# Kernel optimization log

Hardware: AMD Instinct MI355X
Metric: run time of the kernel (lower is better)

Reference implementation:

```python
import jax, jax.numpy as jnp
import numpy as np
import math

D_MODEL = 1024
N_HEAD = 16
D_HEAD = D_MODEL // N_HEAD
SCALE = math.sqrt(D_HEAD)
B, S = 8, 512


def setup_inputs() -> dict:
    key = jax.random.key(0)
    ks = jax.random.split(key, 7)
    x = jax.random.normal(ks[0], (B, S, D_MODEL), dtype=jnp.float32)
    mask = jnp.ones((B, S), dtype=jnp.int32)
    qmask = jax.random.randint(ks[1], (B, S), 0, 2).astype(jnp.int32)
    # params
    Wqkv = jax.random.normal(ks[2], (4 * D_MODEL, D_MODEL), dtype=jnp.float32) / math.sqrt(D_MODEL)
    fc_w = jax.random.normal(ks[3], (D_MODEL, D_MODEL), dtype=jnp.float32) / math.sqrt(D_MODEL)
    fc_b = jnp.zeros((D_MODEL,), dtype=jnp.float32)
    shift = jnp.abs(jax.random.normal(ks[4], (1,), dtype=jnp.float32)) + 0.001
    bias = -jnp.abs(jax.random.normal(ks[5], (1,), dtype=jnp.float32))
    return {"x": x, "mask": mask, "qmask": qmask, "Wqkv": Wqkv,
            "fc_w": fc_w, "fc_b": fc_b, "shift": shift, "bias": bias}


def reference(x, mask, qmask, Wqkv, fc_w, fc_b, shift, bias):
    Bsz, L, D = x.shape
    qkv = x @ Wqkv.T  # [B,S,4D], no bias
    q, k1, k2, v = jnp.split(qkv, 4, axis=-1)

    def heads(t):  # [B,S,D] -> [B,H,S,dh]
        return t.reshape(Bsz, L, N_HEAD, D_HEAD).transpose(0, 2, 1, 3)

    q, k1, k2, v = heads(q), heads(k1), heads(k2), heads(v)

    attn_self = jnp.einsum('bhqd,bhkd->bhqk', q, k1)
    attn_others = jnp.einsum('bhqd,bhkd->bhqk', q, k2)
    same_spk = (qmask[:, :, None] == qmask[:, None, :])[:, None]  # [B,1,S,S]
    attn = jnp.where(same_spk, attn_self, attn_others) / SCALE

    # key padding mask
    attn = jnp.where((mask == 0)[:, None, None, :], -jnp.inf, attn)

    # Gaussian distance bias: -(shift*(i-j)^2 + bias)
    pos = jnp.arange(L, dtype=jnp.float32)
    sq_dist = (pos[:, None] - pos[None, :]) ** 2  # [S,S]
    attn = attn - (shift[0] * sq_dist + bias[0])

    p = jax.nn.softmax(attn, axis=-1)  # dropout=0 (eval)
    out = jnp.einsum('bhqk,bhkd->bhqd', p, v)
    out = out.transpose(0, 2, 1, 3).reshape(Bsz, L, D)
    return out @ fc_w.T + fc_b
```

## Files before the change

kernel.cpp:

```cpp
#include <hip/hip_runtime.h>

typedef unsigned short u16;
typedef __bf16 bf16_t;
typedef bf16_t bf16x8 __attribute__((ext_vector_type(8)));
typedef float f32x4 __attribute__((ext_vector_type(4)));
typedef u16 u16x8 __attribute__((ext_vector_type(8)));
typedef u16 u16x4 __attribute__((ext_vector_type(4)));

__device__ __forceinline__ u16 f2b(float f) {
    unsigned int u = __float_as_uint(f);
    u += 0x7fffu + ((u >> 16) & 1u);
    return (u16)(u >> 16);
}
__device__ __forceinline__ unsigned int pk2(float a, float b) {
    return (unsigned int)f2b(a) | ((unsigned int)f2b(b) << 16);
}

__device__ __forceinline__ f32x4 mfma16(u16x8 a, u16x8 b, f32x4 c) {
    return __builtin_amdgcn_mfma_f32_16x16x32_bf16(
        __builtin_bit_cast(bf16x8, a), __builtin_bit_cast(bf16x8, b), c, 0, 0, 0);
}

#define GLDS16(gp, lp)                                                          \
    __builtin_amdgcn_global_load_lds(                                           \
        (const __attribute__((address_space(1))) void*)(gp),                    \
        (__attribute__((address_space(3))) void*)(lp), 16, 0, 0)

__global__ __launch_bounds__(256) void cvt3_kernel(const float* __restrict__ s0,
                                                   const float* __restrict__ s1,
                                                   const float* __restrict__ s2,
                                                   u16* __restrict__ d0,
                                                   u16* __restrict__ d1,
                                                   u16* __restrict__ d2) {
    int i = (blockIdx.x * 256 + threadIdx.x) * 4;
    const float* src; u16* dst;
    if (i < 4194304)       { src = s0;           dst = d0;           }
    else if (i < 8388608)  { src = s1 - 4194304; dst = d1 - 4194304; }
    else                   { src = s2 - 8388608; dst = d2 - 8388608; }
    float4 f = *(const float4*)(src + i);
    u16x4 o = { f2b(f.x), f2b(f.y), f2b(f.z), f2b(f.w) };
    *(u16x4*)(dst + i) = o;
}

template <int MT, int MODE>
__global__ __launch_bounds__(256) void gemm_bt(
    const u16* __restrict__ A, const u16* __restrict__ Bw,
    u16* __restrict__ Qf, u16* __restrict__ K1f,
    u16* __restrict__ K2f, u16* __restrict__ Vf,
    float* __restrict__ Cf, const float* __restrict__ biasp)
{
    constexpr int K = 1024;
    constexpr int MF = MT / 32;
    __shared__ u16 As[2][MT * 32];
    __shared__ u16 Bs[2][128 * 32];
    const int t = threadIdx.x;
    const int lane = t & 63;
    const int w = t >> 6;
    const int wm = w >> 1, wn = w & 1;
    const int lr = lane & 15, quad = lane >> 4;
    const int tileM = blockIdx.y * MT, tileN = blockIdx.x * 128;

    f32x4 acc[MF][4] = {};

    const u16* Ag = A + (size_t)(tileM + (t >> 2)) * K + (t & 3) * 8;
    const u16* Bg = Bw + (size_t)(tileN + (t >> 2)) * K + (t & 3) * 8;

    const bool swp = (MODE == 0) && (blockIdx.x < 24);
    const u16* Afb = swp ? &Bs[0][0] : &As[0][0];
    const u16* Bfb = swp ? &As[0][0] : &Bs[0][0];
    const int AfS = swp ? 128 * 32 : MT * 32;
    const int BfS = swp ? MT * 32 : 128 * 32;

#define STAGE(kk, bufi)                                                         \
    do {                                                                        \
        GLDS16(Ag + (kk), &As[bufi][t * 8]);                                    \
        if (MT == 128) GLDS16(Ag + (kk) + 64 * K, &As[bufi][t * 8 + 2048]);     \
        GLDS16(Bg + (kk), &Bs[bufi][t * 8]);                                    \
        GLDS16(Bg + (kk) + 64 * K, &Bs[bufi][t * 8 + 2048]);                    \
    } while (0)

    STAGE(0, 0);
    __syncthreads();

#pragma unroll 2
    for (int kk = 0; kk < K; kk += 32) {
        const int cur = (kk >> 5) & 1;
        if (kk + 32 < K) STAGE(kk + 32, cur ^ 1);

        u16x8 af[MF], bf[4];
#pragma unroll
        for (int i = 0; i < MF; ++i)
            af[i] = *(const u16x8*)(Afb + cur * AfS + (wm * (MT / 2) + i * 16 + lr) * 32 + quad * 8);
#pragma unroll
        for (int i = 0; i < 4; ++i)
            bf[i] = *(const u16x8*)(Bfb + cur * BfS + (wn * 64 + i * 16 + lr) * 32 + quad * 8);
#pragma unroll
        for (int mi = 0; mi < MF; ++mi)
#pragma unroll
            for (int ni = 0; ni < 4; ++ni)
                acc[mi][ni] = mfma16(af[mi], bf[ni], acc[mi][ni]);

        __syncthreads();
    }
#undef STAGE

    if (MODE == 0) {
        if (swp) {
            const int kvi = blockIdx.x >> 3;
            const int h = ((blockIdx.x & 7) << 1) + wm;
            const int bh = ((blockIdx.y >> 2) << 4) + h;
            const int t16b = ((blockIdx.y & 3) << 3) + wn * 4;
            u16* bp = (kvi == 0 ? Qf : (kvi == 1 ? K1f : K2f))
                    + ((size_t)(bh * 32 + t16b) * 2) * 512 + lr * 32 + quad * 4;
#pragma unroll
            for (int mi = 0; mi < MF; ++mi)
#pragma unroll
                for (int ni = 0; ni < 4; ++ni) {
                    uint2 v;
                    v.x = pk2(acc[mi][ni][0], acc[mi][ni][1]);
                    v.y = pk2(acc[mi][ni][2], acc[mi][ni][3]);
                    *(uint2*)(bp + ni * 1024 + (mi >> 1) * 512 + (mi & 1) * 16) = v;
                }
        } else {
            const int h = ((blockIdx.x - 24) << 1) + wn;
            const int bh = ((blockIdx.y >> 2) << 4) + h;
            const int t5b = ((blockIdx.y & 3) << 2) + wm * 2;
            u16* bp = Vf + ((size_t)(bh * 4) * 16 + t5b) * 512 + lr * 32 + quad * 4;
#pragma unroll
            for (int mi = 0; mi < MF; ++mi)
#pragma unroll
                for (int ni = 0; ni < 4; ++ni) {
                    uint2 v;
                    v.x = pk2(acc[mi][ni][0], acc[mi][ni][1]);
                    v.y = pk2(acc[mi][ni][2], acc[mi][ni][3]);
                    *(uint2*)(bp + ni * 8192 + (mi >> 1) * 512 + (mi & 1) * 16) = v;
                }
        }
    } else {
#pragma unroll
        for (int mi = 0; mi < MF; ++mi)
#pragma unroll
            for (int ni = 0; ni < 4; ++ni) {
                int n = tileN + wn * 64 + ni * 16 + lr;
                float bv = biasp[n];
#pragma unroll
                for (int r = 0; r < 4; ++r) {
                    int m = tileM + wm * (MT / 2) + mi * 16 + quad * 4 + r;
                    Cf[(size_t)m * 1024 + n] = acc[mi][ni][r] + bv;
                }
            }
    }
}

__global__ __launch_bounds__(256) void attn_kernel(
    const u16* __restrict__ qfm, const u16* __restrict__ k1fm,
    const u16* __restrict__ k2fm, const u16* __restrict__ vfm,
    const int* __restrict__ maskp, const int* __restrict__ qmaskp,
    const float* __restrict__ shiftp, const float* __restrict__ biasp,
    u16* __restrict__ ao)
{
    __shared__ u16 Pw[4][2][512];

    const int bh = blockIdx.x & 127, qt = blockIdx.x >> 7;
    const int b = bh >> 4, h = bh & 15;
    const int t = threadIdx.x, lane = t & 63, w = t >> 6;
    const int lr = lane & 15, quad = lane >> 4;
    const float shiftv = shiftp[0], biasv = biasp[0];

    const int qbase = qt * 128 + w * 32;
    const int m16 = qbase >> 4;
    const int loff = lr * 32 + quad * 8;

    const u16* qb = qfm + ((size_t)(bh * 32 + m16) * 2) * 512 + loff;
    u16x8 qa[2][2];
    qa[0][0] = *(const u16x8*)(qb);
    qa[0][1] = *(const u16x8*)(qb + 512);
    qa[1][0] = *(const u16x8*)(qb + 1024);
    qa[1][1] = *(const u16x8*)(qb + 1536);

    int qmr[2][4]; float rowf[2][4];
#pragma unroll
    for (int g = 0; g < 2; ++g)
#pragma unroll
        for (int r = 0; r < 4; ++r) {
            int m = qbase + g * 16 + quad * 4 + r;
            qmr[g][r] = qmaskp[b * 512 + m];
            rowf[g][r] = (float)m;
        }

    f32x4 o[2][4] = {};
    float lsum[2][4] = {};

    u16* pb[2] = { &Pw[w][0][0], &Pw[w][1][0] };
    const int wa0 = quad * 128 + (((lr >> 3) ^ quad) * 8) + (lr & 7);
    const int wa1 = quad * 128 + (((2 | (lr >> 3)) ^ quad) * 8) + (lr & 7);
    const int ra = lr * 32 + ((quad ^ (lr >> 2)) * 8);

    const u16* k1b = k1fm + (size_t)bh * 32768 + loff;
    const u16* k2b = k2fm + (size_t)bh * 32768 + loff;
    const u16* vb  = vfm  + (size_t)bh * 32768 + loff;
    const int* qmb = qmaskp + b * 512;
    const int* kmb = maskp + b * 512;

#pragma unroll 2
    for (int cc = 0; cc < 16; ++cc) {
        const u16* kc1 = k1b + cc * 2048;
        const u16* kc2 = k2b + cc * 2048;
        u16x8 k1f_[2][2], k2f_[2][2];
        k1f_[0][0] = *(const u16x8*)(kc1);
        k1f_[0][1] = *(const u16x8*)(kc1 + 512);
        k1f_[1][0] = *(const u16x8*)(kc1 + 1024);
        k1f_[1][1] = *(const u16x8*)(kc1 + 1536);
        k2f_[0][0] = *(const u16x8*)(kc2);
        k2f_[0][1] = *(const u16x8*)(kc2 + 512);
        k2f_[1][0] = *(const u16x8*)(kc2 + 1024);
        k2f_[1][1] = *(const u16x8*)(kc2 + 1536);
        u16x8 vf_[4];
#pragma unroll
        for (int ot = 0; ot < 4; ++ot)
            vf_[ot] = *(const u16x8*)(vb + (size_t)(ot * 16 + cc) * 512);

        f32x4 z = {0.f, 0.f, 0.f, 0.f};
        f32x4 s1[2][2], s2[2][2];
#pragma unroll
        for (int g = 0; g < 2; ++g)
#pragma unroll
            for (int tg = 0; tg < 2; ++tg) {
                s1[g][tg] = mfma16(qa[g][1], k1f_[tg][1], mfma16(qa[g][0], k1f_[tg][0], z));
                s2[g][tg] = mfma16(qa[g][1], k2f_[tg][1], mfma16(qa[g][0], k2f_[tg][0], z));
            }

        const int col0 = cc * 32 + lr, col1 = col0 + 16;
        const int qmc0 = qmb[col0], qmc1 = qmb[col1];
        const float ka0 = (kmb[col0] ? 0.f : -1e30f) - 10.0f;
        const float ka1 = (kmb[col1] ? 0.f : -1e30f) - 10.0f;
        const float colf0 = (float)col0, colf1 = (float)col1;

#pragma unroll
        for (int g = 0; g < 2; ++g) {
#pragma unroll
            for (int r = 0; r < 4; ++r) {
                float d0 = rowf[g][r] - colf0;
                float d1 = rowf[g][r] - colf1;
                float sel0 = (qmr[g][r] == qmc0) ? s1[g][0][r] : s2[g][0][r];
                float sel1 = (qmr[g][r] == qmc1) ? s1[g][1][r] : s2[g][1][r];
                float v0 = fmaf(sel0, 0.125f, -fmaf(shiftv * d0, d0, biasv)) + ka0;
                float v1 = fmaf(sel1, 0.125f, -fmaf(shiftv * d1, d1, biasv)) + ka1;
                float p0 = __expf(v0);
                float p1 = __expf(v1);
                lsum[g][r] += p0 + p1;
                pb[g][wa0 + r * 32] = f2b(p0);
                pb[g][wa1 + r * 32] = f2b(p1);
            }
        }
#pragma unroll
        for (int g = 0; g < 2; ++g) {
            u16x8 af = *(const u16x8*)(pb[g] + ra);
#pragma unroll
            for (int ot = 0; ot < 4; ++ot)
                o[g][ot] = mfma16(af, vf_[ot], o[g][ot]);
        }
    }

#pragma unroll
    for (int g = 0; g < 2; ++g)
#pragma unroll
        for (int r = 0; r < 4; ++r) {
            float s = lsum[g][r];
#pragma unroll
            for (int m = 1; m < 16; m <<= 1) s += __shfl_xor(s, m);
            float inv = 1.0f / s;
            int grow = b * 512 + qbase + g * 16 + quad * 4 + r;
            u16* orow = ao + (size_t)grow * 1024 + h * 64 + lr;
            orow[0]  = f2b(o[g][0][r] * inv);
            orow[16] = f2b(o[g][1][r] * inv);
            orow[32] = f2b(o[g][2][r] * inv);
            orow[48] = f2b(o[g][3][r] * inv);
        }
}

extern "C" void kernel_launch(void* const* d_in, const int* in_sizes, int n_in,
                              void* d_out, int out_size, void* d_ws, size_t ws_size,
                              hipStream_t stream) {
    (void)in_sizes; (void)n_in; (void)out_size; (void)ws_size;
    const float* x      = (const float*)d_in[0];
    const int*   maskp  = (const int*)d_in[1];
    const int*   qmaskp = (const int*)d_in[2];
    const float* Wqkv   = (const float*)d_in[3];
    const float* fc_w   = (const float*)d_in[4];
    const float* fc_b   = (const float*)d_in[5];
    const float* shiftp = (const float*)d_in[6];
    const float* biasp  = (const float*)d_in[7];
    float* out = (float*)d_out;

    char* ws = (char*)d_ws;
    u16* xb   = (u16*)(ws);
    u16* wb   = (u16*)(ws + (8u << 20));
    u16* fwb  = (u16*)(ws + (16u << 20));
    u16* qfm  = (u16*)(ws + (18u << 20));
    u16* k1fm = (u16*)(ws + (26u << 20));
    u16* k2fm = (u16*)(ws + (34u << 20));
    u16* vfm  = (u16*)(ws + (42u << 20));
    u16* aob  = (u16*)(ws + (50u << 20));

    cvt3_kernel<<<9216, 256, 0, stream>>>(x, Wqkv, fc_w, xb, wb, fwb);
    gemm_bt<128, 0><<<dim3(32, 32), 256, 0, stream>>>(xb, wb, qfm, k1fm, k2fm, vfm,
                                                      nullptr, nullptr);
    attn_kernel<<<512, 256, 0, stream>>>(qfm, k1fm, k2fm, vfm, maskp, qmaskp,
                                         shiftp, biasp, aob);
    gemm_bt<64, 1><<<dim3(8, 64), 256, 0, stream>>>(aob, fwb, nullptr, nullptr,
                                                    nullptr, nullptr, out, fc_b);
}
```

Before: 204.7 us.

## Replace direct global-to-LDS loads with register-staged double-buffered prefetch in GEMM

Tile loading in the bf16 GEMM changes from global_load_lds into LDS to ordinary global loads into registers, issued two K-steps ahead. The registers are then written to the alternate LDS buffer after each step's MFMAs. The aim is to hide global memory latency behind a deeper prefetch and to keep loads from sitting in the synchronisation path. In exchange it uses more VGPRs for the staging registers and adds explicit LDS store instructions, which may lower occupancy.

Result: no change. 206.2 us (+0.7%).

```diff
diff --git a/kernel.cpp b/kernel.cpp
--- a/kernel.cpp
+++ b/kernel.cpp
@@ -20,11 +20,6 @@
     return __builtin_amdgcn_mfma_f32_16x16x32_bf16(
         __builtin_bit_cast(bf16x8, a), __builtin_bit_cast(bf16x8, b), c, 0, 0, 0);
 }
-
-#define GLDS16(gp, lp)                                                          \
-    __builtin_amdgcn_global_load_lds(                                           \
-        (const __attribute__((address_space(1))) void*)(gp),                    \
-        (__attribute__((address_space(3))) void*)(lp), 16, 0, 0)
 
 __global__ __launch_bounds__(256) void cvt3_kernel(const float* __restrict__ s0,
                                                    const float* __restrict__ s1,
@@ -51,6 +46,7 @@
 {
     constexpr int K = 1024;
     constexpr int MF = MT / 32;
+    constexpr int NA = (MT == 128) ? 2 : 1;
     __shared__ u16 As[2][MT * 32];
     __shared__ u16 Bs[2][128 * 32];
     const int t = threadIdx.x;
@@ -71,38 +67,54 @@
     const int AfS = swp ? 128 * 32 : MT * 32;
     const int BfS = swp ? MT * 32 : 128 * 32;
 
-#define STAGE(kk, bufi)                                                         \
+    u16x8 rA[2][NA], rB[2][2];
+
+#define LOADR(kk, s)                                                            \
     do {                                                                        \
-        GLDS16(Ag + (kk), &As[bufi][t * 8]);                                    \
-        if (MT == 128) GLDS16(Ag + (kk) + 64 * K, &As[bufi][t * 8 + 2048]);     \
-        GLDS16(Bg + (kk), &Bs[bufi][t * 8]);                                    \
-        GLDS16(Bg + (kk) + 64 * K, &Bs[bufi][t * 8 + 2048]);                    \
+        rA[s][0] = *(const u16x8*)(Ag + (kk));                                  \
+        if (NA == 2) rA[s][NA - 1] = *(const u16x8*)(Ag + (kk) + 64 * K);       \
+        rB[s][0] = *(const u16x8*)(Bg + (kk));                                  \
+        rB[s][1] = *(const u16x8*)(Bg + (kk) + 64 * K);                         \
     } while (0)
-
-    STAGE(0, 0);
+#define WRITES(bufi, s)                                                         \
+    do {                                                                        \
+        *(u16x8*)(&As[bufi][t * 8]) = rA[s][0];                                 \
+        if (NA == 2) *(u16x8*)(&As[bufi][t * 8 + 2048]) = rA[s][NA - 1];        \
+        *(u16x8*)(&Bs[bufi][t * 8]) = rB[s][0];                                 \
+        *(u16x8*)(&Bs[bufi][t * 8 + 2048]) = rB[s][1];                          \
+    } while (0)
+
+    LOADR(0, 0);
+    LOADR(32, 1);
+    WRITES(0, 0);
     __syncthreads();
 
 #pragma unroll 2
     for (int kk = 0; kk < K; kk += 32) {
-        const int cur = (kk >> 5) & 1;
-        if (kk + 32 < K) STAGE(kk + 32, cur ^ 1);
+        const int i = kk >> 5;
+        const int cur = i & 1;
+        if (kk + 64 < K) LOADR(kk + 64, cur);
 
         u16x8 af[MF], bf[4];
 #pragma unroll
-        for (int i = 0; i < MF; ++i)
-            af[i] = *(const u16x8*)(Afb + cur * AfS + (wm * (MT / 2) + i * 16 + lr) * 32 + quad * 8);
-#pragma unroll
-        for (int i = 0; i < 4; ++i)
-            bf[i] = *(const u16x8*)(Bfb + cur * BfS + (wn * 64 + i * 16 + lr) * 32 + quad * 8);
+        for (int j = 0; j < MF; ++j)
+            af[j] = *(const u16x8*)(Afb + cur * AfS + (wm * (MT / 2) + j * 16 + lr) * 32 + quad * 8);
+#pragma unroll
+        for (int j = 0; j < 4; ++j)
+            bf[j] = *(const u16x8*)(Bfb + cur * BfS + (wn * 64 + j * 16 + lr) * 32 + quad * 8);
 #pragma unroll
         for (int mi = 0; mi < MF; ++mi)
 #pragma unroll
             for (int ni = 0; ni < 4; ++ni)
                 acc[mi][ni] = mfma16(af[mi], bf[ni], acc[mi][ni]);
 
-        __syncthreads();
+        if (kk + 32 < K) {
+            WRITES(cur ^ 1, cur ^ 1);
+            __syncthreads();
+        }
     }
-#undef STAGE
+#undef LOADR
+#undef WRITES
 
     if (MODE == 0) {
         if (swp) {
```
